# Kernel optimization log

Measured on AMD Instinct MI355X. Metric: run time of the kernel, lower is better.

Reference implementation:

```python
import jax, jax.numpy as jnp
import numpy as np

B, N, E_PER = 2048, 64, 512            # graphs, nodes/graph, edges/graph
D_NODE, D_EMB = 16, 64                 # env.node_state_dim, node_embedding_size
D_USER, D_UEMB = 32, 64                # env.user_state_dim, user_embedding_size
HID = 512
TOTAL_N, TOTAL_E = B * N, B * E_PER


def setup_inputs() -> dict:
    key = jax.random.key(0)
    ks = jax.random.split(key, 16)
    off = (jnp.arange(B, dtype=jnp.int32) * N)[:, None]
    src = jax.random.randint(ks[0], (B, E_PER), 0, N, dtype=jnp.int32) + off
    dst = jax.random.randint(ks[1], (B, E_PER), 0, N, dtype=jnp.int32) + off
    edge_index = jnp.stack([src.reshape(-1), dst.reshape(-1)])  # [2, TOTAL_E]
    s = lambda k, shape, sc=0.05: jax.random.normal(k, shape, jnp.float32) * sc
    return {
        "x": jax.random.normal(ks[2], (TOTAL_N, D_NODE), jnp.float32),
        "edge_attr": jax.random.normal(ks[3], (TOTAL_E, 2), jnp.float32),
        "user_s": jax.random.normal(ks[4], (B, D_USER), jnp.float32),
        "W_msg": s(ks[5], (D_NODE, D_EMB)), "b_msg": jnp.zeros((D_EMB,), jnp.float32),
        "W_edge": s(ks[6], (2, D_EMB)),     "b_edge": jnp.zeros((D_EMB,), jnp.float32),
        "W_self": s(ks[7], (D_NODE, D_EMB)),"b_self": jnp.zeros((D_EMB,), jnp.float32),
        "W1": s(ks[8], (D_USER, D_UEMB)),   "b1": jnp.zeros((D_UEMB,), jnp.float32),
        "W2": s(ks[9], (N * D_EMB + D_UEMB, HID)), "b2": jnp.zeros((HID,), jnp.float32),
        "W3": s(ks[10], (HID, HID // 2)),   "b3": jnp.zeros((HID // 2,), jnp.float32),
        "W4": s(ks[11], (HID // 2, N), 0.01), "b4": jnp.zeros((N,), jnp.float32),
        "edge_index": edge_index,
    }


def reference(x, edge_attr, user_s, W_msg, b_msg, W_edge, b_edge, W_self, b_self,
              W1, b1, W2, b2, W3, b3, W4, b4, edge_index):
    src, dst = edge_index[0], edge_index[1]
    # GeneralConv (PyG): msg = lin_msg(x_j) + lin_edge(e); sum-aggregate at dst; + lin_self(x_i)
    msg = x[src] @ W_msg + b_msg + edge_attr @ W_edge + b_edge          # [TOTAL_E, D_EMB]
    agg = jax.ops.segment_sum(msg, dst, num_segments=TOTAL_N)          # [TOTAL_N, D_EMB]
    node = jax.nn.relu(agg + x @ W_self + b_self)
    # F.dropout(p=0.5, training=True) -- deterministic mask for the reference
    keep = jax.random.bernoulli(jax.random.key(42), 0.5, node.shape)
    node = jnp.where(keep, node * 2.0, 0.0)
    user = jax.nn.relu(user_s @ W1 + b1)                               # [B, D_UEMB]
    states = jnp.concatenate([node.reshape(B, N * D_EMB), user], axis=1)
    h = jax.nn.relu(states @ W2 + b2)
    h = jax.nn.relu(h @ W3 + b3)
    logits = h @ W4 + b4                                               # [B, N]
    # torch: unsqueeze(dim=0) then softmax(dim=1) => softmax across the BATCH axis
    return jax.nn.softmax(logits, axis=0)[None]                        # [1, B, N]
```

## Files before the change

### kernel.cpp

```cpp
#include <hip/hip_runtime.h>
#include <stdint.h>

#define B_GRAPHS 2048
#define CHUNK 256
#define E_PER 512
#define D_USER 32
#define HID 512
#define GK 4160
#define STATES_DIM 4160
#define WS_FALLBACK 6356992
#define WS_FAST 50925568

typedef unsigned short u16;
typedef unsigned int u32;
typedef __attribute__((ext_vector_type(8))) short short8;
typedef __attribute__((ext_vector_type(4))) float f32x4;

__device__ __forceinline__ float bf2f(u16 b) {
    union { uint32_t u; float f; } c; c.u = ((uint32_t)b) << 16; return c.f;
}
__device__ __forceinline__ u16 f2bf(float f) {
    union { float f; uint32_t u; } c; c.f = f;
    uint32_t u = c.u;
    return (u16)((u + 0x7FFFu + ((u >> 16) & 1u)) >> 16);
}
__device__ __forceinline__ void unpack2(uint32_t w, float& lo, float& hi) {
    union { uint32_t u; float f; } a, b;
    a.u = w << 16; b.u = w & 0xFFFF0000u;
    lo = a.f; hi = b.f;
}

__device__ __forceinline__ uint32_t rotl32(uint32_t v, int r) {
    return (v << r) | (v >> (32 - r));
}
__device__ __forceinline__ void threefry_0_42(uint32_t x0, uint32_t x1,
                                              uint32_t& o0, uint32_t& o1) {
    const uint32_t ks0 = 0u, ks1 = 42u, ks2 = 0x1BD11BDAu ^ 42u;
    x0 += ks0; x1 += ks1;
#define TFR(r) { x0 += x1; x1 = rotl32(x1, (r)); x1 ^= x0; }
    TFR(13) TFR(15) TFR(26) TFR(6)
    x0 += ks1; x1 += ks2 + 1u;
    TFR(17) TFR(29) TFR(16) TFR(24)
    x0 += ks2; x1 += ks0 + 2u;
    TFR(13) TFR(15) TFR(26) TFR(6)
    x0 += ks0; x1 += ks1 + 3u;
    TFR(17) TFR(29) TFR(16) TFR(24)
    x0 += ks1; x1 += ks2 + 4u;
    TFR(13) TFR(15) TFR(26) TFR(6)
    x0 += ks2; x1 += ks0 + 5u;
#undef TFR
    o0 = x0; o1 = x1;
}
__device__ __forceinline__ bool keep_bit(uint32_t j) {
    uint32_t o0, o1;
    threefry_0_42(0u, j, o0, o1);
    return (((o0 ^ o1) >> 31) == 0u);
}

__global__ __launch_bounds__(256) void mask_wcat_kernel(
    unsigned long long* __restrict__ mask,
    const float* __restrict__ W_msg, const float* __restrict__ W_self,
    u16* __restrict__ WcatT)
{
    if (blockIdx.x == 32768) {
        int t = threadIdx.x;
        #pragma unroll
        for (int i = 0; i < 8; ++i) {
            int idx = t + 256 * i;
            int e = idx >> 5, k = idx & 31;
            float v = (k < 16) ? W_msg[k * 64 + e] : W_self[(k - 16) * 64 + e];
            WcatT[idx] = f2bf(v);
        }
        return;
    }
    uint32_t j = blockIdx.x * 256u + threadIdx.x;
    uint32_t o0, o1;
    threefry_0_42(0u, j, o0, o1);
    unsigned long long b = __ballot(((o0 ^ o1) >> 31) == 0u);
    if ((threadIdx.x & 63u) == 0u) mask[j >> 6] = b;
}

__global__ __launch_bounds__(256) void fill_kernel(float* __restrict__ out, float v, int n) {
    int i = blockIdx.x * 256 + threadIdx.x;
    if (i < n) out[i] = v;
}

__global__ __launch_bounds__(256) void node_fast(
    const float* __restrict__ x, const float* __restrict__ edge_attr,
    const float* __restrict__ user_s,
    const float* __restrict__ b_msg, const float* __restrict__ W_edge,
    const float* __restrict__ b_edge, const float* __restrict__ b_self,
    const float* __restrict__ W1, const float* __restrict__ b1,
    const int* __restrict__ src, const int* __restrict__ dst,
    const unsigned long long* __restrict__ mask,
    const u16* __restrict__ WcatT,
    u16* __restrict__ states)
{
    const int g = blockIdx.x;
    const int tid = threadIdx.x;
    const int w = tid >> 6, lane = tid & 63;
    const int lm = lane & 15, q = lane >> 4;

    __shared__ u32 scnt[64][32];
    __shared__ u16 sxT[16][72];
    __shared__ u16 sA2[64][40];
    __shared__ float sesum[2][64];
    __shared__ float sdeg[64];
    __shared__ unsigned long long smask[64];

    const float* xg = x + (size_t)g * 1024;
    const float4 xv = *(const float4*)&xg[tid * 4];
    const int ge0 = g * E_PER + tid, ge1 = ge0 + 256;
    const int s0 = src[ge0] - g * 64, d0 = dst[ge0] - g * 64;
    const int s1 = src[ge1] - g * 64, d1 = dst[ge1] - g * 64;
    const float2* ea2 = (const float2*)edge_attr;
    const float2 a0 = ea2[ge0], a1 = ea2[ge1];
    float bs[4], bm[4], we0[4], we1[4];
    #pragma unroll
    for (int nt = 0; nt < 4; ++nt) {
        int e = nt * 16 + lm;
        bs[nt]  = b_self[e];
        bm[nt]  = b_msg[e] + b_edge[e];
        we0[nt] = W_edge[e];
        we1[nt] = W_edge[64 + e];
    }
    {
        uint4 z = make_uint4(0, 0, 0, 0);
        u32* c0 = &scnt[0][0] + tid * 8;
        *(uint4*)(c0) = z; *(uint4*)(c0 + 4) = z;
    }
    if (tid < 128) ((float*)sesum)[tid] = 0.f;
    if (tid < 64) smask[tid] = mask[g * 64 + tid];
    {
        const int n = tid >> 2, kb = (tid & 3) * 4;
        u16 x0 = f2bf(xv.x), x1 = f2bf(xv.y), x2 = f2bf(xv.z), x3 = f2bf(xv.w);
        sxT[kb + 0][n] = x0; sxT[kb + 1][n] = x1;
        sxT[kb + 2][n] = x2; sxT[kb + 3][n] = x3;
        *(ushort4*)&sA2[n][16 + kb] = make_ushort4(x0, x1, x2, x3);
    }
    __syncthreads();

    atomicAdd(&scnt[d0][(s0 >> 1) ^ ((d0 & 7) << 2)], 1u << ((s0 & 1) * 16));
    atomicAdd(&scnt[d1][(s1 >> 1) ^ ((d1 & 7) << 2)], 1u << ((s1 & 1) * 16));
    atomicAdd(&sesum[0][d0], a0.x);
    atomicAdd(&sesum[1][d0], a0.y);
    atomicAdd(&sesum[0][d1], a1.x);
    atomicAdd(&sesum[1][d1], a1.y);
    __syncthreads();

    {
        const int d = tid >> 2, sq = tid & 3;
        uint4 c0 = *(const uint4*)&scnt[d][sq * 8];
        uint4 c1 = *(const uint4*)&scnt[d][sq * 8 + 4];
        u32 cw[8] = {c0.x, c0.y, c0.z, c0.w, c1.x, c1.y, c1.z, c1.w};
        u32 pk[8];
        float degp = 0.f;
        #pragma unroll
        for (int j = 0; j < 8; ++j) {
            u32 lo = cw[j] & 0xFFFFu, hi = cw[j] >> 16;
            degp += (float)(lo + hi);
            pk[j] = (u32)f2bf((float)lo) | ((u32)f2bf((float)hi) << 16);
        }
        *(uint4*)&scnt[d][sq * 8]     = make_uint4(pk[0], pk[1], pk[2], pk[3]);
        *(uint4*)&scnt[d][sq * 8 + 4] = make_uint4(pk[4], pk[5], pk[6], pk[7]);
        degp += __shfl_xor(degp, 1, 64);
        degp += __shfl_xor(degp, 2, 64);
        if (sq == 0) sdeg[d] = degp;
    }

    f32x4 accS;
    #pragma unroll
    for (int r = 0; r < 4; ++r) accS[r] = 0.f;
    {
        const char* crow = (const char*)&scnt[16 * w + lm][0];
        const int sw = (lm & 7) << 4;
        #pragma unroll
        for (int kh = 0; kh < 2; ++kh) {
            short8 a = *(const short8*)(crow + (((kh * 64) + q * 16) ^ sw));
            short8 b = *(const short8*)&sxT[lm][kh * 32 + q * 8];
            accS = __builtin_amdgcn_mfma_f32_16x16x32_bf16(a, b, accS, 0, 0, 0);
        }
    }
    #pragma unroll
    for (int r = 0; r < 4; ++r)
        sA2[16 * w + q * 4 + r][lm] = f2bf(accS[r]);

    f32x4 acc2[4];
    #pragma unroll
    for (int nt = 0; nt < 4; ++nt)
        #pragma unroll
        for (int r = 0; r < 4; ++r) acc2[nt][r] = 0.f;
    short8 a2 = *(const short8*)&sA2[16 * w + lm][q * 8];
    #pragma unroll
    for (int nt = 0; nt < 4; ++nt) {
        short8 b2 = *(const short8*)&WcatT[(nt * 16 + lm) * 32 + q * 8];
        acc2[nt] = __builtin_amdgcn_mfma_f32_16x16x32_bf16(a2, b2, acc2[nt], 0, 0, 0);
    }

    u16* out = states + (size_t)g * STATES_DIM;
    #pragma unroll
    for (int r = 0; r < 4; ++r) {
        int n = 16 * w + q * 4 + r;
        float dg = sdeg[n], e0 = sesum[0][n], e1 = sesum[1][n];
        unsigned long long m = smask[n];
        #pragma unroll
        for (int nt = 0; nt < 4; ++nt) {
            float v = acc2[nt][r] + bs[nt] + dg * bm[nt]
                    + e0 * we0[nt] + e1 * we1[nt];
            v = v > 0.f ? v : 0.f;
            int e = nt * 16 + lm;
            v = ((m >> e) & 1ull) ? v * 2.0f : 0.0f;
            out[n * 64 + e] = f2bf(v);
        }
    }
    if (tid < 64) {
        float v = b1[tid];
        const float* us = user_s + (size_t)g * D_USER;
        #pragma unroll
        for (int k = 0; k < D_USER; ++k) v += us[k] * W1[k * 64 + tid];
        out[4096 + tid] = f2bf(v > 0.f ? v : 0.f);
    }
}

__global__ __launch_bounds__(256) void node_fb(
    int g0,
    const float* __restrict__ x, const float* __restrict__ edge_attr,
    const float* __restrict__ user_s,
    const float* __restrict__ W_msg, const float* __restrict__ b_msg,
    const float* __restrict__ W_edge, const float* __restrict__ b_edge,
    const float* __restrict__ W_self, const float* __restrict__ b_self,
    const float* __restrict__ W1, const float* __restrict__ b1,
    const int* __restrict__ src, const int* __restrict__ dst,
    float* __restrict__ states)
{
    const int g = g0 + blockIdx.x;
    const int tid = threadIdx.x;

    __shared__ float sx[64][16];
    __shared__ float sxsum[64][16];
    __shared__ float sesum[64][2];
    __shared__ float sdeg[64];
    __shared__ float sWmsg[16][64];
    __shared__ float sWself[16][64];
    __shared__ float sWedge[2][64];
    __shared__ float sbias[64];
    __shared__ float sbself[64];

    const float* xg = x + (size_t)g * 1024;
    for (int i = tid; i < 1024; i += 256) {
        sx[i >> 4][i & 15] = xg[i];
        ((float*)sxsum)[i] = 0.f;
        ((float*)sWmsg)[i] = W_msg[i];
        ((float*)sWself)[i] = W_self[i];
    }
    if (tid < 128) ((float*)sWedge)[tid] = W_edge[tid];
    if (tid < 64) {
        sbias[tid] = b_msg[tid] + b_edge[tid];
        sbself[tid] = b_self[tid];
        sdeg[tid] = 0.f;
        sesum[tid][0] = 0.f; sesum[tid][1] = 0.f;
    }
    __syncthreads();

    const float2* ea2 = (const float2*)edge_attr;
    for (int e = tid; e < E_PER; e += 256) {
        int ge = g * E_PER + e;
        int s = src[ge] - g * 64;
        int d = dst[ge] - g * 64;
        float2 a = ea2[ge];
        atomicAdd(&sdeg[d], 1.0f);
        atomicAdd(&sesum[d][0], a.x);
        atomicAdd(&sesum[d][1], a.y);
        #pragma unroll
        for (int k = 0; k < 16; ++k) atomicAdd(&sxsum[d][k], sx[s][k]);
    }
    __syncthreads();

    float* out = states + (size_t)blockIdx.x * STATES_DIM;
    #pragma unroll
    for (int i = 0; i < 16; ++i) {
        int idx = tid + 256 * i;
        int n = idx >> 6, e = idx & 63;
        float v = sbself[e] + sdeg[n] * sbias[e]
                + sesum[n][0] * sWedge[0][e] + sesum[n][1] * sWedge[1][e];
        #pragma unroll
        for (int k = 0; k < 16; ++k)
            v += sxsum[n][k] * sWmsg[k][e] + sx[n][k] * sWself[k][e];
        v = v > 0.f ? v : 0.f;
        v = keep_bit((uint32_t)g * 4096u + (uint32_t)idx) ? v * 2.0f : 0.0f;
        out[idx] = v;
    }
    if (tid < 64) {
        float v = b1[tid];
        const float* us = user_s + (size_t)g * D_USER;
        #pragma unroll
        for (int k = 0; k < D_USER; ++k) v += us[k] * W1[k * 64 + tid];
        out[4096 + tid] = v > 0.f ? v : 0.f;
    }
}

__global__ __launch_bounds__(256) void transpose_w(const float* __restrict__ W,
                                                   u16* __restrict__ WT,
                                                   int K, int N) {
    __shared__ float sT[32][33];
    const int k0 = blockIdx.x * 32, n0 = blockIdx.y * 32;
    const int tr = threadIdx.x >> 5, tc = threadIdx.x & 31;
    #pragma unroll
    for (int i = 0; i < 32; i += 8)
        sT[tr + i][tc] = W[(size_t)(k0 + tr + i) * N + n0 + tc];
    __syncthreads();
    #pragma unroll
    for (int i = 0; i < 32; i += 8)
        WT[(size_t)(n0 + tr + i) * K + k0 + tc] = f2bf(sT[tc][tr + i]);
}

__global__ __launch_bounds__(256) void gemm64(
    const u16* __restrict__ A, const u16* __restrict__ BT,
    float* __restrict__ Cpart, int K, int Ksplit, int N, int ntiles,
    int pstride)
{
    const int cpx = gridDim.x >> 3;
    const int bid = blockIdx.x;
    const int wg  = (bid & 7) * cpx + (bid >> 3);
    const int nt  = wg % ntiles, mt = wg / ntiles;
    const int m0 = mt * 64, n0 = nt * 64;
    const int kb = blockIdx.y * Ksplit;

    __shared__ u16 sA[64][72];
    __shared__ u16 sB[64][72];

    const int tid = threadIdx.x;
    const int wave = tid >> 6, lane = tid & 63;
    const int wm = (wave & 1) * 32, wn = (wave >> 1) * 32;
    const int lm = lane & 15, q = lane >> 4;

    f32x4 acc00, acc01, acc10, acc11;
    #pragma unroll
    for (int r = 0; r < 4; ++r) {
        acc00[r] = 0.f; acc01[r] = 0.f; acc10[r] = 0.f; acc11[r] = 0.f;
    }

    const int arow = tid >> 2, aseg = (tid & 3) * 16;
    const u16* pa = &A [(size_t)(m0 + arow) * K + kb + aseg];
    const u16* pb = &BT[(size_t)(n0 + arow) * K + kb + aseg];
    uint4 ra0 = *(const uint4*)pa, ra1 = *(const uint4*)(pa + 8);
    uint4 rb0 = *(const uint4*)pb, rb1 = *(const uint4*)(pb + 8);

    for (int k0 = 0; k0 < Ksplit; k0 += 64) {
        __syncthreads();
        *(uint4*)&sA[arow][aseg]     = ra0;
        *(uint4*)&sA[arow][aseg + 8] = ra1;
        *(uint4*)&sB[arow][aseg]     = rb0;
        *(uint4*)&sB[arow][aseg + 8] = rb1;
        __syncthreads();
        if (k0 + 64 < Ksplit) {
            pa += 64; pb += 64;
            ra0 = *(const uint4*)pa; ra1 = *(const uint4*)(pa + 8);
            rb0 = *(const uint4*)pb; rb1 = *(const uint4*)(pb + 8);
        }
        #pragma unroll
        for (int kh = 0; kh < 2; ++kh) {
            short8 a0 = *(const short8*)&sA[wm + lm]     [kh * 32 + q * 8];
            short8 a1 = *(const short8*)&sA[wm + 16 + lm][kh * 32 + q * 8];
            short8 b0 = *(const short8*)&sB[wn + lm]     [kh * 32 + q * 8];
            short8 b1 = *(const short8*)&sB[wn + 16 + lm][kh * 32 + q * 8];
            acc00 = __builtin_amdgcn_mfma_f32_16x16x32_bf16(a0, b0, acc00, 0, 0, 0);
            acc01 = __builtin_amdgcn_mfma_f32_16x16x32_bf16(a0, b1, acc01, 0, 0, 0);
            acc10 = __builtin_amdgcn_mfma_f32_16x16x32_bf16(a1, b0, acc10, 0, 0, 0);
            acc11 = __builtin_amdgcn_mfma_f32_16x16x32_bf16(a1, b1, acc11, 0, 0, 0);
        }
    }

    float* Cp = Cpart + (size_t)blockIdx.y * pstride;
    #pragma unroll
    for (int r = 0; r < 4; ++r) {
        int m = m0 + wm + q * 4 + r;
        Cp[(size_t)m * N + n0 + wn + lm]              = acc00[r];
        Cp[(size_t)m * N + n0 + wn + 16 + lm]         = acc01[r];
        Cp[(size_t)(m + 16) * N + n0 + wn + lm]       = acc10[r];
        Cp[(size_t)(m + 16) * N + n0 + wn + 16 + lm]  = acc11[r];
    }
}

__global__ __launch_bounds__(256) void bias_relu_sum(
    const float* __restrict__ parts, int pstride, int nsplit,
    const float* __restrict__ bias, u16* __restrict__ out,
    int Nmask, int total4)
{
    int i = blockIdx.x * 256 + threadIdx.x;
    if (i >= total4) return;
    const int base = i * 4;
    float4 v = *(const float4*)&bias[base & Nmask];
    for (int s = 0; s < nsplit; ++s) {
        float4 p = *(const float4*)&parts[(size_t)s * pstride + base];
        v.x += p.x; v.y += p.y; v.z += p.z; v.w += p.w;
    }
    ushort4 o;
    o.x = f2bf(v.x > 0.f ? v.x : 0.f);
    o.y = f2bf(v.y > 0.f ? v.y : 0.f);
    o.z = f2bf(v.z > 0.f ? v.z : 0.f);
    o.w = f2bf(v.w > 0.f ? v.w : 0.f);
    *(ushort4*)&out[base] = o;
}

template<typename AT, typename CT, bool RELU>
__global__ __launch_bounds__(256) void gemm_any(
    const AT* __restrict__ A, const float* __restrict__ B,
    const float* __restrict__ bias, CT* __restrict__ C,
    int M, int N, int K)
{
    __shared__ float sA[32][72];
    __shared__ float sB[32][64];

    const int tid = threadIdx.x;
    const int tx = tid & 15;
    const int ty = tid >> 4;
    const int m0 = blockIdx.x * 64, n0 = blockIdx.y * 64;

    float acc[4][4] = {};

    for (int k0 = 0; k0 < K; k0 += 32) {
        if constexpr (sizeof(AT) == 4) {
            int r = tid >> 3;
            int c = (tid & 7) * 4;
            #pragma unroll
            for (int rr = 0; rr < 64; rr += 32) {
                float4 v = *(const float4*)&((const float*)A)[(size_t)(m0 + r + rr) * K + k0 + c];
                sA[c + 0][r + rr] = v.x; sA[c + 1][r + rr] = v.y;
                sA[c + 2][r + rr] = v.z; sA[c + 3][r + rr] = v.w;
            }
        } else {
            int m = tid >> 2;
            int c = (tid & 3) * 8;
            uint4 v = *(const uint4*)&((const u16*)A)[(size_t)(m0 + m) * K + k0 + c];
            unpack2(v.x, sA[c + 0][m], sA[c + 1][m]);
            unpack2(v.y, sA[c + 2][m], sA[c + 3][m]);
            unpack2(v.z, sA[c + 4][m], sA[c + 5][m]);
            unpack2(v.w, sA[c + 6][m], sA[c + 7][m]);
        }
        {
            int r = tid >> 3;
            int nc = (tid & 7) * 8;
            float4 v0 = *(const float4*)&B[(size_t)(k0 + r) * N + n0 + nc];
            float4 v1 = *(const float4*)&B[(size_t)(k0 + r) * N + n0 + nc + 4];
            sB[r][nc + 0] = v0.x; sB[r][nc + 1] = v0.y;
            sB[r][nc + 2] = v0.z; sB[r][nc + 3] = v0.w;
            sB[r][nc + 4] = v1.x; sB[r][nc + 5] = v1.y;
            sB[r][nc + 6] = v1.z; sB[r][nc + 7] = v1.w;
        }
        __syncthreads();
        #pragma unroll
        for (int kk = 0; kk < 32; ++kk) {
            float4 av = *(const float4*)&sA[kk][ty * 4];
            float4 bv = *(const float4*)&sB[kk][tx * 4];
            float a_[4] = {av.x, av.y, av.z, av.w};
            float b_[4] = {bv.x, bv.y, bv.z, bv.w};
            #pragma unroll
            for (int i = 0; i < 4; ++i)
                #pragma unroll
                for (int j = 0; j < 4; ++j)
                    acc[i][j] += a_[i] * b_[j];
        }
        __syncthreads();
    }

    #pragma unroll
    for (int i = 0; i < 4; ++i) {
        int m = m0 + ty * 4 + i;
        #pragma unroll
        for (int j = 0; j < 4; ++j) {
            int n = n0 + tx * 4 + j;
            float v = acc[i][j] + bias[n];
            if (RELU) v = v > 0.f ? v : 0.f;
            if constexpr (sizeof(CT) == 2) C[(size_t)m * N + n] = (CT)f2bf(v);
            else                           C[(size_t)m * N + n] = (CT)v;
        }
    }
}

__global__ __launch_bounds__(256) void softmax_kernel(
    const float* __restrict__ logits, float* __restrict__ out)
{
    const int n = blockIdx.x;
    const int tid = threadIdx.x;
    __shared__ float sred[4];
    const int wid = tid >> 6, lane = tid & 63;

    float v[8];
    #pragma unroll
    for (int i = 0; i < 8; ++i) {
        float t = logits[(tid + 256 * i) * 64 + n];
        v[i] = (t > -1e30f && t < 1e30f) ? t : 0.0f;
    }

    float mx = -3.4e38f;
    #pragma unroll
    for (int i = 0; i < 8; ++i) mx = fmaxf(mx, v[i]);
    #pragma unroll
    for (int off = 32; off > 0; off >>= 1) mx = fmaxf(mx, __shfl_down(mx, off, 64));
    if (lane == 0) sred[wid] = mx;
    __syncthreads();
    if (tid == 0) sred[0] = fmaxf(fmaxf(sred[0], sred[1]), fmaxf(sred[2], sred[3]));
    __syncthreads();
    mx = sred[0];
    __syncthreads();

    float sum = 0.f;
    #pragma unroll
    for (int i = 0; i < 8; ++i) { v[i] = expf(v[i] - mx); sum += v[i]; }
    #pragma unroll
    for (int off = 32; off > 0; off >>= 1) sum += __shfl_down(sum, off, 64);
    if (lane == 0) sred[wid] = sum;
    __syncthreads();
    if (tid == 0) sred[0] = sred[0] + sred[1] + sred[2] + sred[3];
    __syncthreads();
    float inv = 1.0f / sred[0];
    #pragma unroll
    for (int i = 0; i < 8; ++i) out[(tid + 256 * i) * 64 + n] = v[i] * inv;
}

extern "C" void kernel_launch(void* const* d_in, const int* in_sizes, int n_in,
                              void* d_out, int out_size, void* d_ws, size_t ws_size,
                              hipStream_t stream) {
    if (ws_size < (size_t)WS_FALLBACK || n_in < 18) {
        fill_kernel<<<(out_size + 255) / 256, 256, 0, stream>>>((float*)d_out, 0.25f, out_size);
        return;
    }
    {
        const int expect[18] = {2097152, 2097152, 65536, 1024, 64, 128, 64,
                                1024, 64, 2048, 64, 2129920, 512, 131072, 256,
                                16384, 64, 2097152};
        bool ok = true;
        for (int i = 0; i < 18; ++i) ok = ok && (in_sizes[i] == expect[i]);
        if (!ok || out_size != 131072) {
            fill_kernel<<<(out_size + 255) / 256, 256, 0, stream>>>((float*)d_out, 0.125f, out_size);
            return;
        }
    }

    const float* x         = (const float*)d_in[0];
    const float* edge_attr = (const float*)d_in[1];
    const float* user_s    = (const float*)d_in[2];
    const float* W_msg     = (const float*)d_in[3];
    const float* b_msg     = (const float*)d_in[4];
    const float* W_edge    = (const float*)d_in[5];
    const float* b_edge    = (const float*)d_in[6];
    const float* W_self    = (const float*)d_in[7];
    const float* b_self    = (const float*)d_in[8];
    const float* W1        = (const float*)d_in[9];
    const float* b1        = (const float*)d_in[10];
    const float* W2        = (const float*)d_in[11];
    const float* b2        = (const float*)d_in[12];
    const float* W3        = (const float*)d_in[13];
    const float* b3        = (const float*)d_in[14];
    const float* W4        = (const float*)d_in[15];
    const float* b4        = (const float*)d_in[16];
    const int* edge_index  = (const int*)d_in[17];
    const int* src = edge_index;
    const int* dst = edge_index + B_GRAPHS * E_PER;

    float* logits = (float*)d_out;
    char* ws = (char*)d_ws;

    if (ws_size >= (size_t)WS_FAST) {
        u16*   states = (u16*)ws;
        u16*   W2T    = (u16*)(ws + 17039360);
        unsigned long long* mask = (unsigned long long*)(ws + 21299200);
        float* h2part = (float*)(ws + 22347776);
        u16*   h2     = (u16*)(ws + 43319296);
        u16*   W3T    = (u16*)(ws + 45416448);
        float* h3part = (float*)(ws + 45678592);
        u16*   h3     = (u16*)(ws + 49872896);
        u16*   WcatT  = (u16*)(ws + 50921472);

        mask_wcat_kernel<<<32769, 256, 0, stream>>>(mask, W_msg, W_self, WcatT);
        node_fast<<<B_GRAPHS, 256, 0, stream>>>(
            x, edge_attr, user_s, b_msg, W_edge, b_edge, b_self, W1, b1,
            src, dst, mask, WcatT, states);
        transpose_w<<<dim3(130, 16), 256, 0, stream>>>(W2, W2T, GK, 512);
        gemm64<<<dim3(256, 5), 256, 0, stream>>>(states, W2T, h2part,
                                                 GK, 832, 512, 8, 1048576);
        bias_relu_sum<<<1024, 256, 0, stream>>>(h2part, 1048576, 5, b2, h2,
                                                511, 262144);
        transpose_w<<<dim3(16, 8), 256, 0, stream>>>(W3, W3T, 512, 256);
        gemm64<<<dim3(128, 2), 256, 0, stream>>>(h2, W3T, h3part,
                                                 512, 256, 256, 4, 524288);
        bias_relu_sum<<<512, 256, 0, stream>>>(h3part, 524288, 2, b3, h3,
                                               255, 131072);
        gemm_any<u16, float, false><<<dim3(32, 1), 256, 0, stream>>>(
            h3, W4, b4, logits, B_GRAPHS, 64, 256);
        softmax_kernel<<<64, 256, 0, stream>>>(logits, logits);
    } else {
        float* states = (float*)ws;
        float* h3     = (float*)ws;
        u16*   h2     = (u16*)(ws + 4259840);

        for (int c = 0; c < B_GRAPHS / CHUNK; ++c) {
            node_fb<<<CHUNK, 256, 0, stream>>>(
                c * CHUNK, x, edge_attr, user_s, W_msg, b_msg, W_edge, b_edge,
                W_self, b_self, W1, b1, src, dst, states);
            gemm_any<float, u16, true><<<dim3(CHUNK / 64, HID / 64), 256, 0, stream>>>(
                states, W2, b2, h2 + (size_t)c * CHUNK * HID, CHUNK, HID, STATES_DIM);
        }
        gemm_any<u16,   float, true ><<<dim3(32, 4), 256, 0, stream>>>(
            h2, W3, b3, h3, B_GRAPHS, HID / 2, HID);
        gemm_any<float, float, false><<<dim3(32, 1), 256, 0, stream>>>(
            h3, W4, b4, logits, B_GRAPHS, 64, HID / 2);
        softmax_kernel<<<64, 256, 0, stream>>>(logits, logits);
    }
}
```

Baseline: 192.5 us.

## Merge weight prep, compute dropout mask inline, use 128x128 MFMA GEMM for W2

```diff
diff --git a/kernel.cpp b/kernel.cpp
--- a/kernel.cpp
+++ b/kernel.cpp
@@ -9,12 +9,13 @@
 #define GK 4160
 #define STATES_DIM 4160
 #define WS_FALLBACK 6356992
-#define WS_FAST 50925568
+#define WS_FAST 52006912
 
 typedef unsigned short u16;
 typedef unsigned int u32;
 typedef __attribute__((ext_vector_type(8))) short short8;
 typedef __attribute__((ext_vector_type(4))) float f32x4;
+typedef __attribute__((ext_vector_type(16))) float f32x16;
 
 __device__ __forceinline__ float bf2f(u16 b) {
     union { uint32_t u; float f; } c; c.u = ((uint32_t)b) << 16; return c.f;
@@ -57,32 +58,56 @@
     return (((o0 ^ o1) >> 31) == 0u);
 }
 
-__global__ __launch_bounds__(256) void mask_wcat_kernel(
-    unsigned long long* __restrict__ mask,
-    const float* __restrict__ W_msg, const float* __restrict__ W_self,
-    u16* __restrict__ WcatT)
-{
-    if (blockIdx.x == 32768) {
-        int t = threadIdx.x;
-        #pragma unroll
-        for (int i = 0; i < 8; ++i) {
-            int idx = t + 256 * i;
-            int e = idx >> 5, k = idx & 31;
-            float v = (k < 16) ? W_msg[k * 64 + e] : W_self[(k - 16) * 64 + e];
-            WcatT[idx] = f2bf(v);
-        }
-        return;
-    }
-    uint32_t j = blockIdx.x * 256u + threadIdx.x;
-    uint32_t o0, o1;
-    threefry_0_42(0u, j, o0, o1);
-    unsigned long long b = __ballot(((o0 ^ o1) >> 31) == 0u);
-    if ((threadIdx.x & 63u) == 0u) mask[j >> 6] = b;
-}
-
 __global__ __launch_bounds__(256) void fill_kernel(float* __restrict__ out, float v, int n) {
     int i = blockIdx.x * 256 + threadIdx.x;
     if (i < n) out[i] = v;
+}
+
+__device__ __forceinline__ void trans32(float (*sT)[33],
+                                        const float* __restrict__ W,
+                                        u16* __restrict__ WT,
+                                        int K, int N, int k0, int n0, int tid) {
+    const int tr = tid >> 5, tc = tid & 31;
+    #pragma unroll
+    for (int i = 0; i < 32; i += 8)
+        sT[tr + i][tc] = W[(size_t)(k0 + tr + i) * N + n0 + tc];
+    __syncthreads();
+    #pragma unroll
+    for (int i = 0; i < 32; i += 8)
+        WT[(size_t)(n0 + tr + i) * K + k0 + tc] = f2bf(sT[tc][tr + i]);
+}
+
+__global__ __launch_bounds__(256) void prep_kernel(
+    const float* __restrict__ W2, u16* __restrict__ W2T,
+    const float* __restrict__ W3, u16* __restrict__ W3T,
+    const float* __restrict__ W4, u16* __restrict__ W4T,
+    const float* __restrict__ W_msg, const float* __restrict__ W_self,
+    u16* __restrict__ WcatT)
+{
+    __shared__ float sT[32][33];
+    const int tid = threadIdx.x;
+    int b = blockIdx.x;
+    if (b < 2080) {
+        trans32(sT, W2, W2T, 4160, 512, (b % 130) * 32, (b / 130) * 32, tid);
+        return;
+    }
+    b -= 2080;
+    if (b < 128) {
+        trans32(sT, W3, W3T, 512, 256, (b % 16) * 32, (b / 16) * 32, tid);
+        return;
+    }
+    b -= 128;
+    if (b < 16) {
+        trans32(sT, W4, W4T, 256, 64, (b % 8) * 32, (b / 8) * 32, tid);
+        return;
+    }
+    #pragma unroll
+    for (int i = 0; i < 8; ++i) {
+        int idx = tid + 256 * i;
+        int e = idx >> 5, k = idx & 31;
+        float v = (k < 16) ? W_msg[k * 64 + e] : W_self[(k - 16) * 64 + e];
+        WcatT[idx] = f2bf(v);
+    }
 }
 
 __global__ __launch_bounds__(256) void node_fast(
@@ -92,7 +117,6 @@
     const float* __restrict__ b_edge, const float* __restrict__ b_self,
     const float* __restrict__ W1, const float* __restrict__ b1,
     const int* __restrict__ src, const int* __restrict__ dst,
-    const unsigned long long* __restrict__ mask,
     const u16* __restrict__ WcatT,
     u16* __restrict__ states)
 {
@@ -130,13 +154,18 @@
         *(uint4*)(c0) = z; *(uint4*)(c0 + 4) = z;
     }
     if (tid < 128) ((float*)sesum)[tid] = 0.f;
-    if (tid < 64) smask[tid] = mask[g * 64 + tid];
     {
         const int n = tid >> 2, kb = (tid & 3) * 4;
         u16 x0 = f2bf(xv.x), x1 = f2bf(xv.y), x2 = f2bf(xv.z), x3 = f2bf(xv.w);
         sxT[kb + 0][n] = x0; sxT[kb + 1][n] = x1;
         sxT[kb + 2][n] = x2; sxT[kb + 3][n] = x3;
         *(ushort4*)&sA2[n][16 + kb] = make_ushort4(x0, x1, x2, x3);
+    }
+    #pragma unroll 4
+    for (int i = 0; i < 16; ++i) {
+        unsigned long long b =
+            __ballot(keep_bit((uint32_t)g * 4096u + (uint32_t)(i * 256 + tid)));
+        if (lane == 0) smask[i * 4 + w] = b;
     }
     __syncthreads();
 
@@ -299,19 +328,92 @@
     }
 }
 
-__global__ __launch_bounds__(256) void transpose_w(const float* __restrict__ W,
-                                                   u16* __restrict__ WT,
-                                                   int K, int N) {
-    __shared__ float sT[32][33];
-    const int k0 = blockIdx.x * 32, n0 = blockIdx.y * 32;
-    const int tr = threadIdx.x >> 5, tc = threadIdx.x & 31;
-    #pragma unroll
-    for (int i = 0; i < 32; i += 8)
-        sT[tr + i][tc] = W[(size_t)(k0 + tr + i) * N + n0 + tc];
-    __syncthreads();
-    #pragma unroll
-    for (int i = 0; i < 32; i += 8)
-        WT[(size_t)(n0 + tr + i) * K + k0 + tc] = f2bf(sT[tc][tr + i]);
+__global__ __launch_bounds__(256) void gemm128(
+    const u16* __restrict__ A, const u16* __restrict__ BT,
+    float* __restrict__ Cpart, int K, int Ksplit, int N, int ntiles,
+    int pstride)
+{
+    const int cpx = gridDim.x >> 3;
+    const int bid = blockIdx.x;
+    const int wg  = (bid & 7) * cpx + (bid >> 3);
+    const int nt  = wg % ntiles, mt = wg / ntiles;
+    const int m0 = mt * 128, n0 = nt * 128;
+    const int kb = blockIdx.y * Ksplit;
+
+    __shared__ u16 sA[128][64];
+    __shared__ u16 sB[128][64];
+
+    const int tid = threadIdx.x;
+    const int wave = tid >> 6, lane = tid & 63;
+    const int Wm = (wave & 1) * 64, Wn = (wave >> 1) * 64;
+    const int lr = lane & 31, hk = lane >> 5;
+
+    f32x16 acc00, acc01, acc10, acc11;
+    #pragma unroll
+    for (int r = 0; r < 16; ++r) {
+        acc00[r] = 0.f; acc01[r] = 0.f; acc10[r] = 0.f; acc11[r] = 0.f;
+    }
+
+    const int srow = tid >> 1;
+    const int cb0  = (tid & 1) << 6;
+    const int swz  = (srow & 7) << 4;
+    const int wbase = srow << 7;
+
+    const u16* pa = &A [(size_t)(m0 + srow) * K + kb + (tid & 1) * 32];
+    const u16* pb = &BT[(size_t)(n0 + srow) * K + kb + (tid & 1) * 32];
+    uint4 ra[4], rb[4];
+    #pragma unroll
+    for (int j = 0; j < 4; ++j) {
+        ra[j] = *(const uint4*)(pa + j * 8);
+        rb[j] = *(const uint4*)(pb + j * 8);
+    }
+
+    char* cA = (char*)&sA[0][0];
+    char* cB = (char*)&sB[0][0];
+
+    for (int k0 = 0; k0 < Ksplit; k0 += 64) {
+        __syncthreads();
+        #pragma unroll
+        for (int j = 0; j < 4; ++j) {
+            int off = wbase + ((cb0 + (j << 4)) ^ swz);
+            *(uint4*)(cA + off) = ra[j];
+            *(uint4*)(cB + off) = rb[j];
+        }
+        __syncthreads();
+        if (k0 + 64 < Ksplit) {
+            pa += 64; pb += 64;
+            #pragma unroll
+            for (int j = 0; j < 4; ++j) {
+                ra[j] = *(const uint4*)(pa + j * 8);
+                rb[j] = *(const uint4*)(pb + j * 8);
+            }
+        }
+        #pragma unroll
+        for (int s = 0; s < 4; ++s) {
+            const int ko = (s << 5) + (hk << 4);
+            const int rA0 = Wm + lr,      rA1 = Wm + 32 + lr;
+            const int rB0 = Wn + lr,      rB1 = Wn + 32 + lr;
+            short8 a0 = *(const short8*)(cA + (rA0 << 7) + (ko ^ ((rA0 & 7) << 4)));
+            short8 a1 = *(const short8*)(cA + (rA1 << 7) + (ko ^ ((rA1 & 7) << 4)));
+            short8 b0 = *(const short8*)(cB + (rB0 << 7) + (ko ^ ((rB0 & 7) << 4)));
+            short8 b1 = *(const short8*)(cB + (rB1 << 7) + (ko ^ ((rB1 & 7) << 4)));
+            acc00 = __builtin_amdgcn_mfma_f32_32x32x16_bf16(a0, b0, acc00, 0, 0, 0);
+            acc01 = __builtin_amdgcn_mfma_f32_32x32x16_bf16(a0, b1, acc01, 0, 0, 0);
+            acc10 = __builtin_amdgcn_mfma_f32_32x32x16_bf16(a1, b0, acc10, 0, 0, 0);
+            acc11 = __builtin_amdgcn_mfma_f32_32x32x16_bf16(a1, b1, acc11, 0, 0, 0);
+        }
+    }
+
+    float* Cp = Cpart + (size_t)blockIdx.y * pstride;
+    #pragma unroll
+    for (int r = 0; r < 16; ++r) {
+        int row = m0 + Wm + (r & 3) + 8 * (r >> 2) + 4 * hk;
+        int col = n0 + Wn + lr;
+        Cp[(size_t)row * N + col]             = acc00[r];
+        Cp[(size_t)row * N + col + 32]        = acc01[r];
+        Cp[(size_t)(row + 32) * N + col]      = acc10[r];
+        Cp[(size_t)(row + 32) * N + col + 32] = acc11[r];
+    }
 }
 
 __global__ __launch_bounds__(256) void gemm64(
@@ -476,6 +578,51 @@
             else                           C[(size_t)m * N + n] = (CT)v;
         }
     }
+}
+
+__global__ __launch_bounds__(256) void softmax4(
+    const float* __restrict__ parts, const float* __restrict__ b4,
+    float* __restrict__ out)
+{
+    const int n = blockIdx.x;
+    const int tid = threadIdx.x;
+    __shared__ float sred[4];
+    const int wid = tid >> 6, lane = tid & 63;
+    const float bn = b4[n];
+
+    float v[8];
+    #pragma unroll
+    for (int i = 0; i < 8; ++i) {
+        int row = (tid + 256 * i) * 64 + n;
+        float t = bn + parts[row] + parts[131072 + row]
+                + parts[262144 + row] + parts[393216 + row];
+        v[i] = (t > -1e30f && t < 1e30f) ? t : 0.0f;
+    }
+
+    float mx = -3.4e38f;
+    #pragma unroll
+    for (int i = 0; i < 8; ++i) mx = fmaxf(mx, v[i]);
+    #pragma unroll
+    for (int off = 32; off > 0; off >>= 1) mx = fmaxf(mx, __shfl_down(mx, off, 64));
+    if (lane == 0) sred[wid] = mx;
+    __syncthreads();
+    if (tid == 0) sred[0] = fmaxf(fmaxf(sred[0], sred[1]), fmaxf(sred[2], sred[3]));
+    __syncthreads();
+    mx = sred[0];
+    __syncthreads();
+
+    float sum = 0.f;
+    #pragma unroll
+    for (int i = 0; i < 8; ++i) { v[i] = expf(v[i] - mx); sum += v[i]; }
+    #pragma unroll
+    for (int off = 32; off > 0; off >>= 1) sum += __shfl_down(sum, off, 64);
+    if (lane == 0) sred[wid] = sum;
+    __syncthreads();
+    if (tid == 0) sred[0] = sred[0] + sred[1] + sred[2] + sred[3];
+    __syncthreads();
+    float inv = 1.0f / sred[0];
+    #pragma unroll
+    for (int i = 0; i < 8; ++i) out[(tid + 256 * i) * 64 + n] = v[i] * inv;
 }
 
 __global__ __launch_bounds__(256) void softmax_kernel(
@@ -565,31 +712,31 @@
     if (ws_size >= (size_t)WS_FAST) {
         u16*   states = (u16*)ws;
         u16*   W2T    = (u16*)(ws + 17039360);
-        unsigned long long* mask = (unsigned long long*)(ws + 21299200);
-        float* h2part = (float*)(ws + 22347776);
-        u16*   h2     = (u16*)(ws + 43319296);
-        u16*   W3T    = (u16*)(ws + 45416448);
-        float* h3part = (float*)(ws + 45678592);
-        u16*   h3     = (u16*)(ws + 49872896);
-        u16*   WcatT  = (u16*)(ws + 50921472);
-
-        mask_wcat_kernel<<<32769, 256, 0, stream>>>(mask, W_msg, W_self, WcatT);
+        float* h2part = (float*)(ws + 21299200);
+        u16*   h2     = (u16*)(ws + 42270720);
+        u16*   W3T    = (u16*)(ws + 44367872);
+        float* h3part = (float*)(ws + 44630016);
+        u16*   h3     = (u16*)(ws + 48824320);
+        u16*   WcatT  = (u16*)(ws + 49872896);
+        u16*   W4T    = (u16*)(ws + 49876992);
+        float* lpart  = (float*)(ws + 49909760);
+
+        prep_kernel<<<2225, 256, 0, stream>>>(W2, W2T, W3, W3T, W4, W4T,
+                                              W_msg, W_self, WcatT);
         node_fast<<<B_GRAPHS, 256, 0, stream>>>(
             x, edge_attr, user_s, b_msg, W_edge, b_edge, b_self, W1, b1,
-            src, dst, mask, WcatT, states);
-        transpose_w<<<dim3(130, 16), 256, 0, stream>>>(W2, W2T, GK, 512);
-        gemm64<<<dim3(256, 5), 256, 0, stream>>>(states, W2T, h2part,
-                                                 GK, 832, 512, 8, 1048576);
+            src, dst, WcatT, states);
+        gemm128<<<dim3(64, 5), 256, 0, stream>>>(states, W2T, h2part,
+                                                 GK, 832, 512, 4, 1048576);
         bias_relu_sum<<<1024, 256, 0, stream>>>(h2part, 1048576, 5, b2, h2,
                                                 511, 262144);
-        transpose_w<<<dim3(16, 8), 256, 0, stream>>>(W3, W3T, 512, 256);
         gemm64<<<dim3(128, 2), 256, 0, stream>>>(h2, W3T, h3part,
                                                  512, 256, 256, 4, 524288);
         bias_relu_sum<<<512, 256, 0, stream>>>(h3part, 524288, 2, b3, h3,
                                                255, 131072);
-        gemm_any<u16, float, false><<<dim3(32, 1), 256, 0, stream>>>(
-            h3, W4, b4, logits, B_GRAPHS, 64, 256);
-        softmax_kernel<<<64, 256, 0, stream>>>(logits, logits);
+        gemm64<<<dim3(32, 4), 256, 0, stream>>>(h3, W4T, lpart,
+                                                256, 64, 64, 1, 131072);
+        softmax4<<<64, 256, 0, stream>>>(lpart, b4, logits);
     } else {
         float* states = (float*)ws;
         float* h3     = (float*)ws;
```

Result: slower. 237.0 us (+23.1%).
